# Performance work log

Hardware: AMD Instinct MI355X
Metric: run time of the kernel (lower is better)

Reference implementation:

```python
import jax, jax.numpy as jnp
import numpy as np

N, E, G = 16384, 65536, 64
IN_F, HID, MID, NCLS = 63, 2048, 1024, 18
EPS = 1e-5
SLOPE = 0.01  # default leaky_relu negative_slope


def setup_inputs() -> dict:
    key = jax.random.key(0)
    ks = jax.random.split(key, 24)
    p = lambda k, shp: jax.random.normal(k, shp, dtype=jnp.float32) * 0.02
    inp = {
        "h": jax.random.normal(ks[0], (N, IN_F), dtype=jnp.float32),
        "src": jax.random.randint(ks[1], (E,), 0, N, dtype=jnp.int32),
        "dst": jax.random.randint(ks[2], (E,), 0, N, dtype=jnp.int32),
        "graph_id": jnp.sort(jax.random.randint(ks[3], (N,), 0, G, dtype=jnp.int32)),
        # SAGEConv layers: fc_self W, fc_neigh W, bias
        "Ws1": p(ks[4], (IN_F, HID)), "Wn1": p(ks[5], (IN_F, HID)), "b1": jnp.zeros((HID,), jnp.float32),
        "Ws2": p(ks[6], (HID, HID)), "Wn2": p(ks[7], (HID, HID)), "b2": jnp.zeros((HID,), jnp.float32),
        "Ws3": p(ks[8], (HID, HID)), "Wn3": p(ks[9], (HID, HID)), "b3": jnp.zeros((HID,), jnp.float32),
        # BatchNorm affine params
        "g1": jnp.ones((HID,), jnp.float32), "be1": jnp.zeros((HID,), jnp.float32),
        "g2": jnp.ones((HID,), jnp.float32), "be2": jnp.zeros((HID,), jnp.float32),
        "g3": jnp.ones((HID,), jnp.float32), "be3": jnp.zeros((HID,), jnp.float32),
        # MLP head
        "fc1_w": p(ks[10], (HID, HID)), "fc1_b": jnp.zeros((HID,), jnp.float32),
        "fc2_w": p(ks[11], (HID, MID)), "fc2_b": jnp.zeros((MID,), jnp.float32),
        "fc3_w": p(ks[12], (MID, NCLS)), "fc3_b": jnp.zeros((NCLS,), jnp.float32),
    }
    return inp


def _sage_mean(h, src, dst, Ws, Wn, b):
    # DGL SAGEConv, aggregator='mean': rst = fc_self(h) + fc_neigh(mean_{u in N(v)} h_u) + bias
    deg = jax.ops.segment_sum(jnp.ones((E,), h.dtype), dst, num_segments=N)
    neigh_sum = jax.ops.segment_sum(h[src], dst, num_segments=N)  # [N, d_in]
    neigh_mean = neigh_sum / jnp.maximum(deg, 1.0)[:, None]       # zero-degree -> 0
    return h @ Ws + neigh_mean @ Wn + b


def _bn(x, gamma, beta):
    # BatchNorm1d in training mode: batch stats over node dim, biased variance
    mu = jnp.mean(x, axis=0)
    var = jnp.mean(jnp.square(x - mu), axis=0)
    return (x - mu) * jax.lax.rsqrt(var + EPS) * gamma + beta


def reference(h, src, dst, graph_id,
              Ws1, Wn1, b1, Ws2, Wn2, b2, Ws3, Wn3, b3,
              g1, be1, g2, be2, g3, be3,
              fc1_w, fc1_b, fc2_w, fc2_b, fc3_w, fc3_b):
    lrelu = lambda x: jax.nn.leaky_relu(x, SLOPE)
    h = lrelu(_bn(_sage_mean(h, src, dst, Ws1, Wn1, b1), g1, be1))
    h = lrelu(_bn(_sage_mean(h, src, dst, Ws2, Wn2, b2), g2, be2))
    h = lrelu(_bn(_sage_mean(h, src, dst, Ws3, Wn3, b3), g3, be3))
    # AvgPooling over batched graph (dropout = identity in eval)
    cnt = jax.ops.segment_sum(jnp.ones((N,), h.dtype), graph_id, num_segments=G)
    hg = jax.ops.segment_sum(h, graph_id, num_segments=G) / jnp.maximum(cnt, 1.0)[:, None]
    x = lrelu(hg @ fc1_w + fc1_b)
    x = lrelu(x @ fc2_w + fc2_b)
    return x @ fc3_w + fc3_b
```

## Files before the change

kernel.cpp:

```cpp
#include <hip/hip_runtime.h>
#include <hip/hip_bf16.h>

#define NN   16384
#define EE   65536
#define GG   64
#define INF  63
#define HID  2048
#define MID  1024
#define NCLS 18
#define EPS  1e-5f
#define SLOPE 0.01f
#define MR   (NN / 128)

typedef unsigned short ushort;
typedef unsigned int uint;

using bf16x8 = __attribute__((ext_vector_type(8))) __bf16;
using f32x4  = __attribute__((ext_vector_type(4))) float;

__device__ __forceinline__ ushort f2us(float x) {
    __hip_bfloat16 b = __float2bfloat16(x);
    return __builtin_bit_cast(ushort, b);
}
__device__ __forceinline__ float us2f(ushort u) {
    return __bfloat162float(__builtin_bit_cast(__hip_bfloat16, u));
}

__device__ __forceinline__ void gll16(const ushort* g, ushort* l) {
    __builtin_amdgcn_global_load_lds(
        (const __attribute__((address_space(1))) uint*)g,
        (__attribute__((address_space(3))) uint*)l, 16, 0, 0);
}


__global__ void k_zero_i(int* __restrict__ p, int n) {
    int i = blockIdx.x * blockDim.x + threadIdx.x;
    if (i < n) p[i] = 0;
}


__global__ void k_count(const int* __restrict__ dst, int* __restrict__ cnt) {
    int e = blockIdx.x * blockDim.x + threadIdx.x;
    if (e < EE) atomicAdd(&cnt[dst[e]], 1);
}

__global__ void k_scan(const int* __restrict__ cnt, int* __restrict__ off,
                       float* __restrict__ deg) {
    __shared__ int sh[1024];
    int t = threadIdx.x;
    int base = t * 16;
    int loc[16];
    int s = 0;
#pragma unroll
    for (int i = 0; i < 16; ++i) {
        int c = cnt[base + i];
        loc[i] = s;
        s += c;
        deg[base + i] = (float)c;
    }
    sh[t] = s;
    __syncthreads();
    for (int d = 1; d < 1024; d <<= 1) {
        int v = (t >= d) ? sh[t - d] : 0;
        __syncthreads();
        sh[t] += v;
        __syncthreads();
    }
    int excl = sh[t] - s;
#pragma unroll
    for (int i = 0; i < 16; ++i) off[base + i] = excl + loc[i];
    if (t == 1023) off[NN] = sh[1023];
}

__global__ void k_fill(const int* __restrict__ src, const int* __restrict__ dst,
                       const int* __restrict__ off, int* __restrict__ cur,
                       int* __restrict__ csr_src) {
    int e = blockIdx.x * blockDim.x + threadIdx.x;
    if (e < EE) {
        int d = dst[e];
        int p = atomicAdd(&cur[d], 1);
        csr_src[off[d] + p] = src[e];
    }
}


__global__ void k_h2bf_c(const float* __restrict__ h, ushort* __restrict__ Xc) {
    int i = blockIdx.x * 256 + threadIdx.x;
    int r = i >> 6, c = i & 63;
    Xc[(size_t)r * 128 + c] = (c < INF) ? f2us(h[(size_t)r * INF + c]) : (ushort)0;
}

__global__ void k_agg_small_c(const float* __restrict__ X, ushort* __restrict__ Xc,
                              const int* __restrict__ off, const int* __restrict__ csr_src,
                              const float* __restrict__ deg) {
    int v = blockIdx.x;
    int f = threadIdx.x;
    float acc = 0.f;
    if (f < INF) {
        int s = off[v], e = off[v + 1];
        for (int i = s; i < e; ++i) acc += X[(size_t)csr_src[i] * INF + f];
        acc /= fmaxf(deg[v], 1.f);
    }
    Xc[(size_t)v * 128 + 64 + f] = f2us(acc);
}


__global__ void k_aggbn(const ushort* __restrict__ Ybf,
                        const float* __restrict__ sc8, const float* __restrict__ sh8,
                        ushort* __restrict__ X, ushort* __restrict__ AggX,
                        const int* __restrict__ off, const int* __restrict__ csr_src,
                        const float* __restrict__ deg) {
    int v = blockIdx.x;
    int t = threadIdx.x;
    int c = t * 8;
    float sc[8], sh[8];
    *(float4*)&sc[0] = *(const float4*)&sc8[c];
    *(float4*)&sc[4] = *(const float4*)&sc8[c + 4];
    *(float4*)&sh[0] = *(const float4*)&sh8[c];
    *(float4*)&sh[4] = *(const float4*)&sh8[c + 4];

    {
        uint4 u = ((const uint4*)(Ybf + (size_t)v * HID))[t];
        uint wds[4] = {u.x, u.y, u.z, u.w};
        uint o[4];
#pragma unroll
        for (int j = 0; j < 4; ++j) {
            float a = sc[2 * j] * us2f((ushort)(wds[j] & 0xffffu)) + sh[2 * j];
            float b = sc[2 * j + 1] * us2f((ushort)(wds[j] >> 16)) + sh[2 * j + 1];
            a = a > 0.f ? a : SLOPE * a;
            b = b > 0.f ? b : SLOPE * b;
            o[j] = (uint)f2us(a) | ((uint)f2us(b) << 16);
        }
        ((uint4*)(X + (size_t)v * HID))[t] = make_uint4(o[0], o[1], o[2], o[3]);
    }

    int s = off[v], e = off[v + 1];
    float acc[8];
#pragma unroll
    for (int j = 0; j < 8; ++j) acc[j] = 0.f;
    for (int i = s; i < e; ++i) {
        uint4 u = ((const uint4*)(Ybf + (size_t)csr_src[i] * HID))[t];
        uint wds[4] = {u.x, u.y, u.z, u.w};
#pragma unroll
        for (int j = 0; j < 4; ++j) {
            float a = sc[2 * j] * us2f((ushort)(wds[j] & 0xffffu)) + sh[2 * j];
            float b = sc[2 * j + 1] * us2f((ushort)(wds[j] >> 16)) + sh[2 * j + 1];
            acc[2 * j]     += a > 0.f ? a : SLOPE * a;
            acc[2 * j + 1] += b > 0.f ? b : SLOPE * b;
        }
    }
    float inv = 1.f / fmaxf(deg[v], 1.f);
    uint o[4];
#pragma unroll
    for (int j = 0; j < 4; ++j)
        o[j] = (uint)f2us(acc[2 * j] * inv) | ((uint)f2us(acc[2 * j + 1] * inv) << 16);
    ((uint4*)(AggX + (size_t)v * HID))[t] = make_uint4(o[0], o[1], o[2], o[3]);
}


__global__ void k_wt2(const float* __restrict__ W0, const float* __restrict__ W1,
                      int K, int N, ushort* __restrict__ Wt0, ushort* __restrict__ Wt1,
                      int Kp) {
    const float* W = blockIdx.z ? W1 : W0;
    ushort* Wt = blockIdx.z ? Wt1 : Wt0;
    __shared__ float t[32][33];
    int kb = blockIdx.y * 32, nb = blockIdx.x * 32;
    int tx = threadIdx.x & 31, ty = threadIdx.x >> 5;
#pragma unroll
    for (int i = 0; i < 32; i += 8) {
        int k = kb + ty + i;
        t[ty + i][tx] = (k < K) ? W[(size_t)k * N + nb + tx] : 0.f;
// ... 14 lines not shown
#pragma unroll
    for (int i = 0; i < 32; i += 8) {
        int k = kb + ty + i;
        t[ty + i][tx] = (k < Kw) ? W[(size_t)k * N + nb + tx] : 0.f;
    }
    __syncthreads();
#pragma unroll
    for (int i = 0; i < 32; i += 8)
        Wtc[(size_t)(nb + ty + i) * KP + kOff + kb + tx] = f2us(t[tx][ty + i]);
}

__global__ void k_wt(const float* __restrict__ W, int K, int N,
                     ushort* __restrict__ Wt, int Kp) {
    __shared__ float t[32][33];
    int kb = blockIdx.y * 32, nb = blockIdx.x * 32;
    int tx = threadIdx.x & 31, ty = threadIdx.x >> 5;
#pragma unroll
    for (int i = 0; i < 32; i += 8) {
        int k = kb + ty + i;
        t[ty + i][tx] = (k < K) ? W[(size_t)k * N + nb + tx] : 0.f;
    }
    __syncthreads();
#pragma unroll
    for (int i = 0; i < 32; i += 8)
        Wt[(size_t)(nb + ty + i) * Kp + kb + tx] = f2us(t[tx][ty + i]);
}


#define BK 64

__global__ __launch_bounds__(256)
void k_mgemm(const ushort* __restrict__ A1, int lda1, const ushort* __restrict__ B1t, int ldb1, int K1,
             const ushort* __restrict__ A2, int lda2, const ushort* __restrict__ B2t, int ldb2, int K2,
             const float* __restrict__ bias, float* __restrict__ Cf, ushort* __restrict__ Cbf,
             int ldc, int fuse_lrelu, float* __restrict__ s1p, float* __restrict__ s2p,
             size_t cStrideZ) {
    __shared__ __align__(16) ushort As[128 * BK];
    __shared__ __align__(16) ushort Bs[128 * BK];
    __shared__ float sb1[4][64];
    __shared__ float sb2[4][64];
    const int tid = threadIdx.x;
    const int lane = tid & 63;
    const int w = tid >> 6;
    const int rowBase = blockIdx.y * 128;
    const int colBase = blockIdx.x * 128;
    const int m0 = (w & 1) * 64;
    const int n0 = (w >> 1) * 64;
    const int z = blockIdx.z;
    A1 += (size_t)z * K1;
    B1t += (size_t)z * K1;
    if (Cf) Cf += (size_t)z * cStrideZ;

    f32x4 acc[4][4];
#pragma unroll
    for (int mi = 0; mi < 4; ++mi)
#pragma unroll
        for (int ni = 0; ni < 4; ++ni) acc[mi][ni] = (f32x4){0.f, 0.f, 0.f, 0.f};

    const int lrow = w * 8 + (lane >> 3);
    const int gc8 = ((lane & 7) ^ (lane >> 3)) * 8;
    const int la = lane & 15, q = lane >> 4;
    const int la7 = lane & 7;

    for (int pass = 0; pass < 2; ++pass) {
        const ushort* A  = pass ? A2 : A1;
        const ushort* Bt = pass ? B2t : B1t;
        const int K   = pass ? K2 : K1;
        const int lda = pass ? lda2 : lda1;
        const int ldb = pass ? ldb2 : ldb1;
        if (A == nullptr) continue;
        const ushort* gA = A + (size_t)(rowBase + lrow) * lda + gc8;
        const ushort* gB = Bt + (size_t)(colBase + lrow) * ldb + gc8;
        for (int kt = 0; kt < K; kt += BK) {
#pragma unroll
            for (int j = 0; j < 4; ++j) {
                gll16(gA + (size_t)(j * 32) * lda + kt, As + j * 2048 + w * 512);
                gll16(gB + (size_t)(j * 32) * ldb + kt, Bs + j * 2048 + w * 512);
            }
            __syncthreads();
#pragma unroll
            for (int kk = 0; kk < 2; ++kk) {
                const int lc8 = ((kk * 4 + q) ^ la7) * 8;
                bf16x8 av[4], bv[4];
#pragma unroll
                for (int mi = 0; mi < 4; ++mi)
                    av[mi] = *(const bf16x8*)&As[(m0 + mi * 16 + la) * BK + lc8];
#pragma unroll
                for (int ni = 0; ni < 4; ++ni)
                    bv[ni] = *(const bf16x8*)&Bs[(n0 + ni * 16 + la) * BK + lc8];
#pragma unroll
                for (int mi = 0; mi < 4; ++mi)
#pragma unroll
                    for (int ni = 0; ni < 4; ++ni)
                        acc[mi][ni] = __builtin_amdgcn_mfma_f32_16x16x32_bf16(
                            av[mi], bv[ni], acc[mi][ni], 0, 0, 0);
            }
            __syncthreads();
        }
    }

#pragma unroll
    for (int mi = 0; mi < 4; ++mi) {
#pragma unroll
        for (int ni = 0; ni < 4; ++ni) {
            const int lc = colBase + n0 + ni * 16 + la;
            const float bv = bias ? bias[lc] : 0.f;
#pragma unroll
            for (int r = 0; r < 4; ++r) {
                const int row = rowBase + m0 + mi * 16 + q * 4 + r;
                float v = acc[mi][ni][r] + bv;
                if (fuse_lrelu) v = v > 0.f ? v : SLOPE * v;
                if (Cbf) Cbf[(size_t)row * ldc + lc] = f2us(v);
                else     Cf[(size_t)row * ldc + lc] = v;
            }
        }
    }

    if (s1p) {
#pragma unroll
        for (int ni = 0; ni < 4; ++ni) {
            const int lc = colBase + n0 + ni * 16 + la;
            const float bv = bias ? bias[lc] : 0.f;
            float t1 = 0.f, t2 = 0.f;
#pragma unroll
            for (int mi = 0; mi < 4; ++mi)
#pragma unroll
                for (int r = 0; r < 4; ++r) {
                    float v = acc[mi][ni][r] + bv;
                    t1 += v;
                    t2 += v * v;
                }
            t1 += __shfl_xor(t1, 16);
            t1 += __shfl_xor(t1, 32);
            t2 += __shfl_xor(t2, 16);
            t2 += __shfl_xor(t2, 32);
            if (q == 0) {
                sb1[w][ni * 16 + la] = t1;
                sb2[w][ni * 16 + la] = t2;
            }
        }
        __syncthreads();
        if (tid < 128) {
            int half = tid >> 6, j = tid & 63;
            float v1 = sb1[2 * half][j] + sb1[2 * half + 1][j];
            float v2 = sb2[2 * half][j] + sb2[2 * half + 1][j];
            size_t o = (size_t)blockIdx.y * ldc + colBase + half * 64 + j;
            s1p[o] = v1;
            s2p[o] = v2;
        }
    }
}


#define STAGEH(kti_, wh_) do {                                                 \
    int _kt = (kti_);                                                          \
    int _ktc = _kt < KT ? _kt : KT - 1;                                        \
    int _pass = (_ktc >= kt1);                                                 \
    int _k0 = (_ktc - (_pass ? kt1 : 0)) << 6;                                 \
    const ushort* _M;                                                          \
    int _h, _slot;                                                             \
    if ((wh_) == 0)      { _M = (_pass ? A2 : A1) + (size_t)rowBase * HID; _h = 0; _slot = 0; } \
    else if ((wh_) == 2) { _M = (_pass ? A2 : A1) + (size_t)rowBase * HID; _h = 1; _slot = 1; } \
    else if ((wh_) == 1) { _M = (_pass ? B2t : B1t) + (size_t)colBase * HID; _h = 0; _slot = 2; } \
    else                 { _M = (_pass ? B2t : B1t) + (size_t)colBase * HID; _h = 1; _slot = 3; } \
    const ushort* _g = _M + (size_t)(_h * 128 + srow) * HID + (size_t)(_k0 + sch); \
    ushort* _l = &lds[_kt & 1][_slot][0] + ldsl;                               \
    gll16(_g, _l);                                                             \
    gll16(_g + (size_t)64 * HID, _l + 4096);                                   \
} while (0)

#define PHASE(buf_, hm_, hn_, loadB_, skti_, swh_, wait_) do {                 \
    const ushort* _Ah = &lds[(buf_)][(hm_)][0];                                \
    if (loadB_) {                                                              \
        const ushort* _Bh = &lds[(buf_)][2 + (hn_)][0];                        \
        _Pragma("unroll")                                                      \
        for (int g_ = 0; g_ < 2; ++g_) {                                       \
            b[g_][0] = *(const bf16x8*)&_Bh[brb + g_ * 4096 + c0];             \
            b[g_][1] = *(const bf16x8*)&_Bh[brb + g_ * 4096 + c1];             \
        }                                                                      \
    }                                                                          \
    _Pragma("unroll")                                                          \
    for (int f_ = 0; f_ < 4; ++f_) {                                           \
        a[f_][0] = *(const bf16x8*)&_Ah[arb + f_ * 2048 + c0];                 \
        a[f_][1] = *(const bf16x8*)&_Ah[arb + f_ * 2048 + c1];                 \
    }                                                                          \
    STAGEH((skti_), (swh_));                                                   \
    __builtin_amdgcn_s_barrier();                                              \
    __builtin_amdgcn_s_setprio(1);                                             \
    _Pragma("unroll")                                                          \
    for (int kk_ = 0; kk_ < 2; ++kk_)                                          \
        _Pragma("unroll")                                                      \
        for (int f_ = 0; f_ < 4; ++f_)                                         \
            _Pragma("unroll")                                                  \
            for (int g_ = 0; g_ < 2; ++g_)                                     \
                acc[(hm_) * 4 + f_][(hn_) * 2 + g_] =                          \
                    __builtin_amdgcn_mfma_f32_16x16x32_bf16(                   \
                        a[f_][kk_], b[g_][kk_],                                \
                        acc[(hm_) * 4 + f_][(hn_) * 2 + g_], 0, 0, 0);         \
    __builtin_amdgcn_s_setprio(0);                                             \
    if (wait_) asm volatile("s_waitcnt vmcnt(6)" ::: "memory");                \
    __builtin_amdgcn_s_barrier();                                              \
} while (0)

__global__ __launch_bounds__(512, 2)
void k_mgemm256(const ushort* __restrict__ A1, const ushort* __restrict__ B1t,
                const ushort* __restrict__ A2, const ushort* __restrict__ B2t,
                int K1, int K2,
                const float* __restrict__ bias, ushort* __restrict__ Cbf,
                float* __restrict__ s1p, float* __restrict__ s2p) {
    __shared__ __align__(16) ushort lds[2][4][128 * 64];
    __shared__ float sb1[2][256];
    __shared__ float sb2[2][256];

    const int tid  = threadIdx.x;
    const int w    = tid >> 6, lane = tid & 63;
    const int la   = lane & 15, q = lane >> 4, la7 = lane & 7;
    const int wm   = w >> 2, wn = w & 3;

    const int nx  = gridDim.x;
    const int lin = blockIdx.y * nx + blockIdx.x;
    const int cpx = (nx * gridDim.y) >> 3;
    const int swz = (lin & 7) * cpx + (lin >> 3);
    const int bx  = swz & (nx - 1), by = swz / nx;
    const int rowBase = by * 256, colBase = bx * 256;

    const int kt1 = K1 >> 6;
    const int KT  = kt1 + (K2 >> 6);

    const int srow = tid >> 3;
    const int sch  = ((tid & 7) ^ (srow & 7)) << 3;
    const int ldsl = w << 9;

    const int arb = (wm * 16 + la) * 64;
    const int brb = (wn * 16 + la) * 64;
    const int c0  = ((0 + q) ^ la7) << 3;
    const int c1  = ((4 + q) ^ la7) << 3;

    f32x4 acc[8][4];
#pragma unroll
    for (int mi = 0; mi < 8; ++mi)
#pragma unroll
        for (int ni = 0; ni < 4; ++ni) acc[mi][ni] = (f32x4){0.f, 0.f, 0.f, 0.f};
    bf16x8 a[4][2], b[2][2];

    STAGEH(0, 0); STAGEH(0, 1); STAGEH(0, 2); STAGEH(0, 3);
    STAGEH(1, 0);
    asm volatile("s_waitcnt vmcnt(6)" ::: "memory");
    __builtin_amdgcn_s_barrier();

    for (int t = 0; t < KT; ++t) {
        const int bf_ = t & 1;
        PHASE(bf_, 0, 0, 1, t + 1, 1, 1);
        PHASE(bf_, 1, 0, 0, t + 1, 2, 1);
        PHASE(bf_, 0, 1, 1, t + 1, 3, 0);
        PHASE(bf_, 1, 1, 0, t + 2, 0, 1);
    }

    __syncthreads();

#pragma unroll
    for (int mi = 0; mi < 8; ++mi) {
        const int row = rowBase + (mi >> 2) * 128 + wm * 16 + (mi & 3) * 32 + q * 4;
#pragma unroll
        for (int ni = 0; ni < 4; ++ni) {
            const int col = colBase + (ni >> 1) * 128 + wn * 16 + (ni & 1) * 64 + la;
            const float bv = bias[col];
#pragma unroll
            for (int r = 0; r < 4; ++r) {
                float v = acc[mi][ni][r] + bv;
                Cbf[(size_t)(row + r) * HID + col] = f2us(v);
            }
        }
    }

#pragma unroll
    for (int ni = 0; ni < 4; ++ni) {
        const int cib = (ni >> 1) * 128 + wn * 16 + (ni & 1) * 64 + la;
        const float bv = bias[colBase + cib];
        float t1 = 0.f, t2 = 0.f;
#pragma unroll
        for (int mi = 0; mi < 8; ++mi)
#pragma unroll
            for (int r = 0; r < 4; ++r) {
                float v = acc[mi][ni][r] + bv;
                t1 += v;
                t2 += v * v;
            }
        t1 += __shfl_xor(t1, 16);
        t1 += __shfl_xor(t1, 32);
        t2 += __shfl_xor(t2, 16);
        t2 += __shfl_xor(t2, 32);
        if (q == 0) { sb1[wm][cib] = t1; sb2[wm][cib] = t2; }
    }
    __syncthreads();
    if (tid < 256) {
        size_t o = (size_t)by * HID + colBase + tid;
        s1p[o] = sb1[0][tid] + sb1[1][tid];
        s2p[o] = sb2[0][tid] + sb2[1][tid];
    }
}


__global__ void k_bn_finalize(const float* __restrict__ p1, const float* __restrict__ p2,
                              const float* __restrict__ gamma, const float* __restrict__ beta,
                              float* __restrict__ scale, float* __restrict__ shift, int nrb) {
    int c = blockIdx.x * 256 + threadIdx.x;
    if (c >= HID) return;
    float s1 = 0.f, s2 = 0.f;
    for (int rb = 0; rb < nrb; ++rb) {
        s1 += p1[(size_t)rb * HID + c];
        s2 += p2[(size_t)rb * HID + c];
    }
    float mean = s1 * (1.f / (float)NN);
    float var = s2 * (1.f / (float)NN) - mean * mean;
    var = fmaxf(var, 0.f);
    float sc = gamma[c] * rsqrtf(var + EPS);
    scale[c] = sc;
    shift[c] = beta[c] - mean * sc;
}


__global__ void k_poolbn(const ushort* __restrict__ Ybf,
                         const float* __restrict__ scale, const float* __restrict__ shift,
                         const int* __restrict__ gstart, ushort* __restrict__ hgbf) {
    int g = blockIdx.y;
    int col = blockIdx.x * 256 + threadIdx.x;
    if (g >= GG) {
        hgbf[(size_t)g * HID + col] = 0;
        return;
    }
    int s = gstart[g], e = gstart[g + 1];
    float sc = scale[col], sh = shift[col];
    float acc = 0.f;
    for (int n = s; n < e; ++n) {
        float v = sc * us2f(Ybf[(size_t)n * HID + col]) + sh;
        acc += v > 0.f ? v : SLOPE * v;
    }
    hgbf[(size_t)g * HID + col] = f2us(acc / fmaxf((float)(e - s), 1.f));
}

__global__ void k_gstart(const int* __restrict__ gid, int* __restrict__ gstart) {
    int g = threadIdx.x;
    if (g > GG) return;
    int lo = 0, hi = NN;
    while (lo < hi) {
        int mid = (lo + hi) >> 1;
        if (gid[mid] < g) lo = mid + 1; else hi = mid;
    }
    gstart[g] = lo;
}


__global__ void k_redhead(const float* __restrict__ part, int P, size_t strideZ,
                          const float* __restrict__ bias, int ldc,
                          ushort* __restrict__ obf, float* __restrict__ of, int n) {
    int i = blockIdx.x * 256 + threadIdx.x;
    if (i >= n) return;
    float s = 0.f;
    for (int p = 0; p < P; ++p) s += part[(size_t)p * strideZ + i];
    s += bias[i % ldc];
    s = s > 0.f ? s : SLOPE * s;
    if (obf) obf[i] = f2us(s);
    else     of[i] = s;
}

__global__ void k_fc3(const float* __restrict__ x2, const float* __restrict__ W,
                      const float* __restrict__ b, float* __restrict__ out) {
    int g = blockIdx.x;
    int tid = threadIdx.x;
    float part[NCLS];
#pragma unroll
    for (int c = 0; c < NCLS; ++c) part[c] = 0.f;
    for (int k = tid; k < MID; k += 256) {
        float x = x2[(size_t)g * MID + k];
        const float* wr = W + (size_t)k * NCLS;
#pragma unroll
        for (int c = 0; c < NCLS; ++c) part[c] += x * wr[c];
    }
    __shared__ float red[4][NCLS];
    int lane = tid & 63, w = tid >> 6;
#pragma unroll
    for (int c = 0; c < NCLS; ++c) {
        float v = part[c];
        for (int o = 32; o > 0; o >>= 1) v += __shfl_down(v, o, 64);
        if (lane == 0) red[w][c] = v;
    }
    __syncthreads();
    if (tid < NCLS)
        out[(size_t)g * NCLS + tid] = red[0][tid] + red[1][tid] + red[2][tid] + red[3][tid] + b[tid];
}


extern "C" void kernel_launch(void* const* d_in, const int* in_sizes, int n_in,
                              void* d_out, int out_size, void* d_ws, size_t ws_size,
                              hipStream_t stream) {
    const float* h        = (const float*)d_in[0];
    const int*   src      = (const int*)d_in[1];
    const int*   dst      = (const int*)d_in[2];
    const int*   graph_id = (const int*)d_in[3];
    const float* Ws1 = (const float*)d_in[4];
    const float* Wn1 = (const float*)d_in[5];
    const float* b1  = (const float*)d_in[6];
    const float* Ws2 = (const float*)d_in[7];
    const float* Wn2 = (const float*)d_in[8];
    const float* b2  = (const float*)d_in[9];
    const float* Ws3 = (const float*)d_in[10];
    const float* Wn3 = (const float*)d_in[11];
    const float* b3  = (const float*)d_in[12];
    const float* g1  = (const float*)d_in[13];
    const float* be1 = (const float*)d_in[14];
    const float* g2  = (const float*)d_in[15];
    const float* be2 = (const float*)d_in[16];
    const float* g3  = (const float*)d_in[17];
    const float* be3 = (const float*)d_in[18];
    const float* fc1_w = (const float*)d_in[19];
    const float* fc1_b = (const float*)d_in[20];
    const float* fc2_w = (const float*)d_in[21];
    const float* fc2_b = (const float*)d_in[22];
    const float* fc3_w = (const float*)d_in[23];
    const float* fc3_b = (const float*)d_in[24];
    float* out = (float*)d_out;

    size_t off_b = 0;
    auto alloc = [&](size_t bytes) -> void* {
        void* p = (char*)d_ws + off_b;
        off_b += (bytes + 255) & ~(size_t)255;
        return p;
    };
    ushort* Wt0    = (ushort*)alloc((size_t)2 * HID * HID * 2);
    ushort* Wt1    = Wt0 + (size_t)HID * HID;
    ushort* X      = (ushort*)alloc((size_t)NN * HID * 2);
    ushort* AggX   = (ushort*)alloc((size_t)NN * HID * 2);
    ushort* Ybf    = (ushort*)alloc((size_t)NN * HID * 2);
    float*  deg    = (float*)alloc((size_t)NN * 4);
    int*    csroff = (int*)alloc((size_t)(NN + 1) * 4);
    int*    cursor = (int*)alloc((size_t)NN * 4);
    int*    csrsrc = (int*)alloc((size_t)EE * 4);
    float*  p1     = (float*)alloc((size_t)MR * HID * 4);
    float*  p2     = (float*)alloc((size_t)MR * HID * 4);
    float*  bnsc   = (float*)alloc((size_t)HID * 4);
    float*  bnsh   = (float*)alloc((size_t)HID * 4);
    int*    gstart = (int*)alloc((size_t)(GG + 1) * 4);

    ushort* Xc128 = X;
    ushort* hgbf  = AggX;
    ushort* x1bf  = AggX + (size_t)128 * HID;
    float*  x2f   = (float*)(AggX + (size_t)2 * 128 * HID);
    float*  partF = (float*)(AggX + (size_t)3 * 128 * HID);

    k_zero_i<<<dim3(NN / 256), dim3(256), 0, stream>>>(cursor, NN);
    k_count<<<dim3(EE / 256), dim3(256), 0, stream>>>(dst, cursor);
    k_scan<<<dim3(1), dim3(1024), 0, stream>>>(cursor, csroff, deg);
    k_zero_i<<<dim3(NN / 256), dim3(256), 0, stream>>>(cursor, NN);
    k_fill<<<dim3(EE / 256), dim3(256), 0, stream>>>(src, dst, csroff, cursor, csrsrc);
    k_gstart<<<dim3(1), dim3(128), 0, stream>>>(graph_id, gstart);

    k_h2bf_c<<<dim3(NN * 64 / 256), dim3(256), 0, stream>>>(h, Xc128);
    k_agg_small_c<<<dim3(NN), dim3(64), 0, stream>>>(h, Xc128, csroff, csrsrc, deg);
    k_wt2c<<<dim3(HID / 32, 2, 2), dim3(256), 0, stream>>>(Ws1, Wn1, INF, HID, Wt0, 128);
    k_mgemm<<<dim3(HID / 128, NN / 128, 1), dim3(256), 0, stream>>>(
        Xc128, 128, Wt0, 128, 128,
        (const ushort*)nullptr, 0, (const ushort*)nullptr, 0, 0,
        b1, (float*)nullptr, Ybf, HID, 0, p1, p2, 0);
    k_bn_finalize<<<dim3(HID / 256), dim3(256), 0, stream>>>(p1, p2, g1, be1, bnsc, bnsh, MR);
    k_aggbn<<<dim3(NN), dim3(256), 0, stream>>>(Ybf, bnsc, bnsh, X, AggX, csroff, csrsrc, deg);

    k_wt2<<<dim3(HID / 32, HID / 32, 2), dim3(256), 0, stream>>>(Ws2, Wn2, HID, HID, Wt0, Wt1, HID);
    k_mgemm256<<<dim3(HID / 256, NN / 256), dim3(512), 0, stream>>>(
        X, Wt0, AggX, Wt1, HID, HID, b2, Ybf, p1, p2);
    k_bn_finalize<<<dim3(HID / 256), dim3(256), 0, stream>>>(p1, p2, g2, be2, bnsc, bnsh, NN / 256);
    k_aggbn<<<dim3(NN), dim3(256), 0, stream>>>(Ybf, bnsc, bnsh, X, AggX, csroff, csrsrc, deg);

    k_wt2<<<dim3(HID / 32, HID / 32, 2), dim3(256), 0, stream>>>(Ws3, Wn3, HID, HID, Wt0, Wt1, HID);
    k_mgemm256<<<dim3(HID / 256, NN / 256), dim3(512), 0, stream>>>(
        X, Wt0, AggX, Wt1, HID, HID, b3, Ybf, p1, p2);
    k_bn_finalize<<<dim3(HID / 256), dim3(256), 0, stream>>>(p1, p2, g3, be3, bnsc, bnsh, NN / 256);

    k_poolbn<<<dim3(HID / 256, 128), dim3(256), 0, stream>>>(Ybf, bnsc, bnsh, gstart, hgbf);

    k_wt<<<dim3(HID / 32, HID / 32), dim3(256), 0, stream>>>(fc1_w, HID, HID, Wt0, HID);
    k_wt<<<dim3(MID / 32, HID / 32), dim3(256), 0, stream>>>(fc2_w, HID, MID, Wt1, HID);
    k_mgemm<<<dim3(HID / 128, 1, 4), dim3(256), 0, stream>>>(
        hgbf, HID, Wt0, HID, HID / 4,
        (const ushort*)nullptr, 0, (const ushort*)nullptr, 0, 0,
        (const float*)nullptr, partF, (ushort*)nullptr, HID, 0,
        (float*)nullptr, (float*)nullptr, (size_t)128 * HID);
    k_redhead<<<dim3(128 * HID / 256), dim3(256), 0, stream>>>(
        partF, 4, (size_t)128 * HID, fc1_b, HID, x1bf, (float*)nullptr, 128 * HID);
    k_mgemm<<<dim3(MID / 128, 1, 4), dim3(256), 0, stream>>>(
        x1bf, HID, Wt1, HID, HID / 4,
        (const ushort*)nullptr, 0, (const ushort*)nullptr, 0, 0,
        (const float*)nullptr, partF, (ushort*)nullptr, MID, 0,
        (float*)nullptr, (float*)nullptr, (size_t)128 * MID);
    k_redhead<<<dim3(128 * MID / 256), dim3(256), 0, stream>>>(
        partF, 4, (size_t)128 * MID, fc2_b, MID, (ushort*)nullptr, x2f, 128 * MID);
    k_fc3<<<dim3(GG), dim3(256), 0, stream>>>(x2f, fc3_w, fc3_b, out);
}
```

Baseline: 1.118 ms.

## Switch main GEMM from 16x16x32 to 32x32x16 MFMA tiles

Rewrites the inner loop of the fused SAGE GEMM to use 32x32x16 bf16 MFMA instructions with a per-wave 64x32 sub-tile instead of 16x16x32 fragments. A and B fragments are loaded once per k-tile and reused across the four phases, and the epilogue and BN statistics reduction are remapped to the 32x32 accumulator layout. The aim is fewer LDS reads per flop and higher MFMA throughput per instruction. In exchange, register pressure rises because it holds more fragments at launch bounds of 512 threads with 2 blocks per SM.

After: 1.083 ms. 3.1% less time.

```diff
diff --git a/kernel.cpp b/kernel.cpp
--- a/kernel.cpp
+++ b/kernel.cpp
@@ -17,6 +17,7 @@
 
 using bf16x8 = __attribute__((ext_vector_type(8))) __bf16;
 using f32x4  = __attribute__((ext_vector_type(4))) float;
+using f32x16 = __attribute__((ext_vector_type(16))) float;
 
 __device__ __forceinline__ ushort f2us(float x) {
     __hip_bfloat16 b = __float2bfloat16(x);
@@ -354,39 +355,6 @@
     gll16(_g + (size_t)64 * HID, _l + 4096);                                   \
 } while (0)
 
-#define PHASE(buf_, hm_, hn_, loadB_, skti_, swh_, wait_) do {                 \
-    const ushort* _Ah = &lds[(buf_)][(hm_)][0];                                \
-    if (loadB_) {                                                              \
-        const ushort* _Bh = &lds[(buf_)][2 + (hn_)][0];                        \
-        _Pragma("unroll")                                                      \
-        for (int g_ = 0; g_ < 2; ++g_) {                                       \
-            b[g_][0] = *(const bf16x8*)&_Bh[brb + g_ * 4096 + c0];             \
-            b[g_][1] = *(const bf16x8*)&_Bh[brb + g_ * 4096 + c1];             \
-        }                                                                      \
-    }                                                                          \
-    _Pragma("unroll")                                                          \
-    for (int f_ = 0; f_ < 4; ++f_) {                                           \
-        a[f_][0] = *(const bf16x8*)&_Ah[arb + f_ * 2048 + c0];                 \
-        a[f_][1] = *(const bf16x8*)&_Ah[arb + f_ * 2048 + c1];                 \
-    }                                                                          \
-    STAGEH((skti_), (swh_));                                                   \
-    __builtin_amdgcn_s_barrier();                                              \
-    __builtin_amdgcn_s_setprio(1);                                             \
-    _Pragma("unroll")                                                          \
-    for (int kk_ = 0; kk_ < 2; ++kk_)                                          \
-        _Pragma("unroll")                                                      \
-        for (int f_ = 0; f_ < 4; ++f_)                                         \
-            _Pragma("unroll")                                                  \
-            for (int g_ = 0; g_ < 2; ++g_)                                     \
-                acc[(hm_) * 4 + f_][(hn_) * 2 + g_] =                          \
-                    __builtin_amdgcn_mfma_f32_16x16x32_bf16(                   \
-                        a[f_][kk_], b[g_][kk_],                                \
-                        acc[(hm_) * 4 + f_][(hn_) * 2 + g_], 0, 0, 0);         \
-    __builtin_amdgcn_s_setprio(0);                                             \
-    if (wait_) asm volatile("s_waitcnt vmcnt(6)" ::: "memory");                \
-    __builtin_amdgcn_s_barrier();                                              \
-} while (0)
-
 __global__ __launch_bounds__(512, 2)
 void k_mgemm256(const ushort* __restrict__ A1, const ushort* __restrict__ B1t,
                 const ushort* __restrict__ A2, const ushort* __restrict__ B2t,
@@ -399,7 +367,7 @@
 
     const int tid  = threadIdx.x;
     const int w    = tid >> 6, lane = tid & 63;
-    const int la   = lane & 15, q = lane >> 4, la7 = lane & 7;
+    const int la31 = lane & 31, hi = lane >> 5, la7 = lane & 7;
     const int wm   = w >> 2, wn = w & 3;
 
     const int nx  = gridDim.x;
@@ -416,17 +384,19 @@
     const int sch  = ((tid & 7) ^ (srow & 7)) << 3;
     const int ldsl = w << 9;
 
-    const int arb = (wm * 16 + la) * 64;
-    const int brb = (wn * 16 + la) * 64;
-    const int c0  = ((0 + q) ^ la7) << 3;
-    const int c1  = ((4 + q) ^ la7) << 3;
-
-    f32x4 acc[8][4];
-#pragma unroll
-    for (int mi = 0; mi < 8; ++mi)
-#pragma unroll
-        for (int ni = 0; ni < 4; ++ni) acc[mi][ni] = (f32x4){0.f, 0.f, 0.f, 0.f};
-    bf16x8 a[4][2], b[2][2];
+    const int aoff = (wm * 64 + la31) * 64;
+    const int boff = (wn * 32 + la31) * 64;
+    int cofs[4];
+#pragma unroll
+    for (int s_ = 0; s_ < 4; ++s_)
+        cofs[s_] = (((s_ * 2 + hi) ^ la7) << 3);
+
+    f32x16 acc[8];
+#pragma unroll
+    for (int i = 0; i < 8; ++i)
+#pragma unroll
+        for (int r = 0; r < 16; ++r) acc[i][r] = 0.f;
+    bf16x8 aL[2][4], aH[2][4], bL[4], bH[4];
 
     STAGEH(0, 0); STAGEH(0, 1); STAGEH(0, 2); STAGEH(0, 3);
     STAGEH(1, 0);
@@ -435,47 +405,112 @@
 
     for (int t = 0; t < KT; ++t) {
         const int bf_ = t & 1;
-        PHASE(bf_, 0, 0, 1, t + 1, 1, 1);
-        PHASE(bf_, 1, 0, 0, t + 1, 2, 1);
-        PHASE(bf_, 0, 1, 1, t + 1, 3, 0);
-        PHASE(bf_, 1, 1, 0, t + 2, 0, 1);
+        const ushort* A0h = &lds[bf_][0][0];
+        const ushort* A1h = &lds[bf_][1][0];
+        const ushort* B0h = &lds[bf_][2][0];
+        const ushort* B1h = &lds[bf_][3][0];
+
+#pragma unroll
+        for (int m_ = 0; m_ < 2; ++m_)
+#pragma unroll
+            for (int s_ = 0; s_ < 4; ++s_)
+                aL[m_][s_] = *(const bf16x8*)&A0h[aoff + m_ * 2048 + cofs[s_]];
+#pragma unroll
+        for (int s_ = 0; s_ < 4; ++s_)
+            bL[s_] = *(const bf16x8*)&B0h[boff + cofs[s_]];
+        STAGEH(t + 1, 1);
+        __builtin_amdgcn_s_barrier();
+        __builtin_amdgcn_s_setprio(1);
+#pragma unroll
+        for (int s_ = 0; s_ < 4; ++s_)
+#pragma unroll
+            for (int m_ = 0; m_ < 2; ++m_)
+                acc[m_ * 2] = __builtin_amdgcn_mfma_f32_32x32x16_bf16(
+                    aL[m_][s_], bL[s_], acc[m_ * 2], 0, 0, 0);
+        __builtin_amdgcn_s_setprio(0);
+        asm volatile("s_waitcnt vmcnt(6)" ::: "memory");
+        __builtin_amdgcn_s_barrier();
+
+#pragma unroll
+        for (int m_ = 0; m_ < 2; ++m_)
+#pragma unroll
+            for (int s_ = 0; s_ < 4; ++s_)
+                aH[m_][s_] = *(const bf16x8*)&A1h[aoff + m_ * 2048 + cofs[s_]];
+        STAGEH(t + 1, 2);
+        __builtin_amdgcn_s_barrier();
+        __builtin_amdgcn_s_setprio(1);
+#pragma unroll
+        for (int s_ = 0; s_ < 4; ++s_)
+#pragma unroll
+            for (int m_ = 0; m_ < 2; ++m_)
+                acc[4 + m_ * 2] = __builtin_amdgcn_mfma_f32_32x32x16_bf16(
+                    aH[m_][s_], bL[s_], acc[4 + m_ * 2], 0, 0, 0);
+        __builtin_amdgcn_s_setprio(0);
+        asm volatile("s_waitcnt vmcnt(6)" ::: "memory");
+        __builtin_amdgcn_s_barrier();
+
+#pragma unroll
+        for (int s_ = 0; s_ < 4; ++s_)
+            bH[s_] = *(const bf16x8*)&B1h[boff + cofs[s_]];
+        STAGEH(t + 1, 3);
+        __builtin_amdgcn_s_barrier();
+        __builtin_amdgcn_s_setprio(1);
+#pragma unroll
+        for (int s_ = 0; s_ < 4; ++s_)
+#pragma unroll
+            for (int m_ = 0; m_ < 2; ++m_)
+                acc[1 + m_ * 2] = __builtin_amdgcn_mfma_f32_32x32x16_bf16(
+                    aL[m_][s_], bH[s_], acc[1 + m_ * 2], 0, 0, 0);
+        __builtin_amdgcn_s_setprio(0);
+        __builtin_amdgcn_s_barrier();
+
+        STAGEH(t + 2, 0);
+        __builtin_amdgcn_s_barrier();
+        __builtin_amdgcn_s_setprio(1);
+#pragma unroll
+        for (int s_ = 0; s_ < 4; ++s_)
+#pragma unroll
+            for (int m_ = 0; m_ < 2; ++m_)
+                acc[5 + m_ * 2] = __builtin_amdgcn_mfma_f32_32x32x16_bf16(
+                    aH[m_][s_], bH[s_], acc[5 + m_ * 2], 0, 0, 0);
+        __builtin_amdgcn_s_setprio(0);
+        asm volatile("s_waitcnt vmcnt(6)" ::: "memory");
+        __builtin_amdgcn_s_barrier();
     }
 
     __syncthreads();
 
 #pragma unroll
-    for (int mi = 0; mi < 8; ++mi) {
-        const int row = rowBase + (mi >> 2) * 128 + wm * 16 + (mi & 3) * 32 + q * 4;
-#pragma unroll
-        for (int ni = 0; ni < 4; ++ni) {
-            const int col = colBase + (ni >> 1) * 128 + wn * 16 + (ni & 1) * 64 + la;
+    for (int mt = 0; mt < 4; ++mt) {
+        const int rb = rowBase + (mt >> 1) * 128 + wm * 64 + (mt & 1) * 32 + hi * 4;
+#pragma unroll
+        for (int nt = 0; nt < 2; ++nt) {
+            const int col = colBase + nt * 128 + wn * 32 + la31;
             const float bv = bias[col];
 #pragma unroll
-            for (int r = 0; r < 4; ++r) {
-                float v = acc[mi][ni][r] + bv;
-                Cbf[(size_t)(row + r) * HID + col] = f2us(v);
+            for (int r = 0; r < 16; ++r) {
+                const int row = rb + (r & 3) + (r >> 2) * 8;
+                Cbf[(size_t)row * HID + col] = f2us(acc[mt * 2 + nt][r] + bv);
             }
         }
     }
 
 #pragma unroll
-    for (int ni = 0; ni < 4; ++ni) {
-        const int cib = (ni >> 1) * 128 + wn * 16 + (ni & 1) * 64 + la;
-        const float bv = bias[colBase + cib];
+    for (int nt = 0; nt < 2; ++nt) {
+        const int cl = nt * 128 + wn * 32 + la31;
+        const float bv = bias[colBase + cl];
         float t1 = 0.f, t2 = 0.f;
 #pragma unroll
-        for (int mi = 0; mi < 8; ++mi)
-#pragma unroll
-            for (int r = 0; r < 4; ++r) {
-                float v = acc[mi][ni][r] + bv;
+        for (int mt = 0; mt < 4; ++mt)
+#pragma unroll
+            for (int r = 0; r < 16; ++r) {
+                float v = acc[mt * 2 + nt][r] + bv;
                 t1 += v;
                 t2 += v * v;
             }
-        t1 += __shfl_xor(t1, 16);
         t1 += __shfl_xor(t1, 32);
-        t2 += __shfl_xor(t2, 16);
         t2 += __shfl_xor(t2, 32);
-        if (q == 0) { sb1[wm][cib] = t1; sb2[wm][cib] = t2; }
+        if (hi == 0) { sb1[wm][cl] = t1; sb2[wm][cl] = t2; }
     }
     __syncthreads();
     if (tid < 256) {
```

## Keep A fragments in registers across GEMM phases and use running staging pointers

Applied to the files above, without the earlier changes.

Restructures the main loop of the 256x256 bf16 GEMM so that the low and high A fragments are each read from LDS once per k-tile and kept in registers for two MFMA phases, instead of being re-read in every phase. The per-stage global address computation (clamping, pass selection, branch on half) is replaced by four incrementing pointers, with a one-time jump from the first operand pair to the second at the K1 boundary. The loop is unrolled by two so LDS buffer indices become compile-time constants. This cuts LDS traffic and scalar address math, at the cost of more live VGPRs. It also drops the clamp on the last prefetch, so the final tiles can issue loads past the valid K range.

Result: faster. 1.064 ms (-4.8%).

```diff
diff --git a/kernel.cpp b/kernel.cpp
--- a/kernel.cpp
+++ b/kernel.cpp
@@ -337,54 +337,99 @@
 }
 
 
-#define STAGEH(kti_, wh_) do {                                                 \
-    int _kt = (kti_);                                                          \
-    int _ktc = _kt < KT ? _kt : KT - 1;                                        \
-    int _pass = (_ktc >= kt1);                                                 \
-    int _k0 = (_ktc - (_pass ? kt1 : 0)) << 6;                                 \
-    const ushort* _M;                                                          \
-    int _h, _slot;                                                             \
-    if ((wh_) == 0)      { _M = (_pass ? A2 : A1) + (size_t)rowBase * HID; _h = 0; _slot = 0; } \
-    else if ((wh_) == 2) { _M = (_pass ? A2 : A1) + (size_t)rowBase * HID; _h = 1; _slot = 1; } \
-    else if ((wh_) == 1) { _M = (_pass ? B2t : B1t) + (size_t)colBase * HID; _h = 0; _slot = 2; } \
-    else                 { _M = (_pass ? B2t : B1t) + (size_t)colBase * HID; _h = 1; _slot = 3; } \
-    const ushort* _g = _M + (size_t)(_h * 128 + srow) * HID + (size_t)(_k0 + sch); \
-    ushort* _l = &lds[_kt & 1][_slot][0] + ldsl;                               \
-    gll16(_g, _l);                                                             \
-    gll16(_g + (size_t)64 * HID, _l + 4096);                                   \
+#define STG(ptr_, dst_) do {                                                   \
+    gll16((ptr_), (dst_) + ldsl);                                              \
+    gll16((ptr_) + (size_t)64 * HID, (dst_) + ldsl + 4096);                    \
 } while (0)
 
-#define PHASE(buf_, hm_, hn_, loadB_, skti_, swh_, wait_) do {                 \
-    const ushort* _Ah = &lds[(buf_)][(hm_)][0];                                \
-    if (loadB_) {                                                              \
-        const ushort* _Bh = &lds[(buf_)][2 + (hn_)][0];                        \
-        _Pragma("unroll")                                                      \
-        for (int g_ = 0; g_ < 2; ++g_) {                                       \
-            b[g_][0] = *(const bf16x8*)&_Bh[brb + g_ * 4096 + c0];             \
-            b[g_][1] = *(const bf16x8*)&_Bh[brb + g_ * 4096 + c1];             \
-        }                                                                      \
+#define DO_TILE(BUF) do {                                                      \
+    if (tcur + 1 == kt1) { rB0 += dB; rA1 += dA; rB1 += dB; }                  \
+    if (tcur + 2 == kt1) { rA0 += dA; }                                        \
+    const ushort* A0h = &lds[BUF][0][0];                                       \
+    const ushort* A1h = &lds[BUF][1][0];                                       \
+    const ushort* B0h = &lds[BUF][2][0];                                       \
+    const ushort* B1h = &lds[BUF][3][0];                                       \
+                                                             \
+    _Pragma("unroll")                                                          \
+    for (int f_ = 0; f_ < 4; ++f_) {                                           \
+        aL[f_][0] = *(const bf16x8*)&A0h[arb + f_ * 2048 + c0];                \
+        aL[f_][1] = *(const bf16x8*)&A0h[arb + f_ * 2048 + c1];                \
     }                                                                          \
     _Pragma("unroll")                                                          \
-    for (int f_ = 0; f_ < 4; ++f_) {                                           \
-        a[f_][0] = *(const bf16x8*)&_Ah[arb + f_ * 2048 + c0];                 \
-        a[f_][1] = *(const bf16x8*)&_Ah[arb + f_ * 2048 + c1];                 \
+    for (int g_ = 0; g_ < 2; ++g_) {                                           \
+        bL[g_][0] = *(const bf16x8*)&B0h[brb + g_ * 4096 + c0];                \
+        bL[g_][1] = *(const bf16x8*)&B0h[brb + g_ * 4096 + c1];                \
     }                                                                          \
-    STAGEH((skti_), (swh_));                                                   \
+    STG(rB0, &lds[(BUF) ^ 1][2][0]);                                           \
     __builtin_amdgcn_s_barrier();                                              \
     __builtin_amdgcn_s_setprio(1);                                             \
     _Pragma("unroll")                                                          \
-    for (int kk_ = 0; kk_ < 2; ++kk_)                                          \
+    for (int kk = 0; kk < 2; ++kk)                                             \
         _Pragma("unroll")                                                      \
         for (int f_ = 0; f_ < 4; ++f_)                                         \
             _Pragma("unroll")                                                  \
             for (int g_ = 0; g_ < 2; ++g_)                                     \
-                acc[(hm_) * 4 + f_][(hn_) * 2 + g_] =                          \
-                    __builtin_amdgcn_mfma_f32_16x16x32_bf16(                   \
-                        a[f_][kk_], b[g_][kk_],                                \
-                        acc[(hm_) * 4 + f_][(hn_) * 2 + g_], 0, 0, 0);         \
+                acc[f_][g_] = __builtin_amdgcn_mfma_f32_16x16x32_bf16(         \
+                    aL[f_][kk], bL[g_][kk], acc[f_][g_], 0, 0, 0);             \
     __builtin_amdgcn_s_setprio(0);                                             \
-    if (wait_) asm volatile("s_waitcnt vmcnt(6)" ::: "memory");                \
+    asm volatile("s_waitcnt vmcnt(6)" ::: "memory");                           \
     __builtin_amdgcn_s_barrier();                                              \
+                                                             \
+    _Pragma("unroll")                                                          \
+    for (int f_ = 0; f_ < 4; ++f_) {                                           \
+        aH[f_][0] = *(const bf16x8*)&A1h[arb + f_ * 2048 + c0];                \
+        aH[f_][1] = *(const bf16x8*)&A1h[arb + f_ * 2048 + c1];                \
+    }                                                                          \
+    STG(rA1, &lds[(BUF) ^ 1][1][0]);                                           \
+    __builtin_amdgcn_s_barrier();                                              \
+    __builtin_amdgcn_s_setprio(1);                                             \
+    _Pragma("unroll")                                                          \
+    for (int kk = 0; kk < 2; ++kk)                                             \
+        _Pragma("unroll")                                                      \
+        for (int f_ = 0; f_ < 4; ++f_)                                         \
+            _Pragma("unroll")                                                  \
+            for (int g_ = 0; g_ < 2; ++g_)                                     \
+                acc[4 + f_][g_] = __builtin_amdgcn_mfma_f32_16x16x32_bf16(     \
+                    aH[f_][kk], bL[g_][kk], acc[4 + f_][g_], 0, 0, 0);         \
+    __builtin_amdgcn_s_setprio(0);                                             \
+    asm volatile("s_waitcnt vmcnt(6)" ::: "memory");                           \
+    __builtin_amdgcn_s_barrier();                                              \
+                                                             \
+    _Pragma("unroll")                                                          \
+    for (int g_ = 0; g_ < 2; ++g_) {                                           \
+        bH[g_][0] = *(const bf16x8*)&B1h[brb + g_ * 4096 + c0];                \
+        bH[g_][1] = *(const bf16x8*)&B1h[brb + g_ * 4096 + c1];                \
+    }                                                                          \
+    STG(rB1, &lds[(BUF) ^ 1][3][0]);                                           \
+    __builtin_amdgcn_s_barrier();                                              \
+    __builtin_amdgcn_s_setprio(1);                                             \
+    _Pragma("unroll")                                                          \
+    for (int kk = 0; kk < 2; ++kk)                                             \
+        _Pragma("unroll")                                                      \
+        for (int f_ = 0; f_ < 4; ++f_)                                         \
+            _Pragma("unroll")                                                  \
+            for (int g_ = 0; g_ < 2; ++g_)                                     \
+                acc[f_][2 + g_] = __builtin_amdgcn_mfma_f32_16x16x32_bf16(     \
+                    aL[f_][kk], bH[g_][kk], acc[f_][2 + g_], 0, 0, 0);         \
+    __builtin_amdgcn_s_setprio(0);                                             \
+    __builtin_amdgcn_s_barrier();                                              \
+                                                             \
+    STG(rA0, &lds[BUF][0][0]);                                                 \
+    __builtin_amdgcn_s_barrier();                                              \
+    __builtin_amdgcn_s_setprio(1);                                             \
+    _Pragma("unroll")                                                          \
+    for (int kk = 0; kk < 2; ++kk)                                             \
+        _Pragma("unroll")                                                      \
+        for (int f_ = 0; f_ < 4; ++f_)                                         \
+            _Pragma("unroll")                                                  \
+            for (int g_ = 0; g_ < 2; ++g_)                                     \
+                acc[4 + f_][2 + g_] = __builtin_amdgcn_mfma_f32_16x16x32_bf16( \
+                    aH[f_][kk], bH[g_][kk], acc[4 + f_][2 + g_], 0, 0, 0);     \
+    __builtin_amdgcn_s_setprio(0);                                             \
+    asm volatile("s_waitcnt vmcnt(6)" ::: "memory");                           \
+    __builtin_amdgcn_s_barrier();                                              \
+    rA0 += 64; rB0 += 64; rA1 += 64; rB1 += 64;                                \
+    ++tcur;                                                                    \
 } while (0)
 
 __global__ __launch_bounds__(512, 2)
@@ -416,6 +461,13 @@
     const int sch  = ((tid & 7) ^ (srow & 7)) << 3;
     const int ldsl = w << 9;
 
+    const ushort* rA0 = A1 + (size_t)(rowBase + srow) * HID + sch;
+    const ushort* rA1 = A1 + (size_t)(rowBase + 128 + srow) * HID + sch;
+    const ushort* rB0 = B1t + (size_t)(colBase + srow) * HID + sch;
+    const ushort* rB1 = B1t + (size_t)(colBase + 128 + srow) * HID + sch;
+    const ptrdiff_t dA = (A2 - A1) - K1;
+    const ptrdiff_t dB = (B2t - B1t) - K1;
+
     const int arb = (wm * 16 + la) * 64;
     const int brb = (wn * 16 + la) * 64;
     const int c0  = ((0 + q) ^ la7) << 3;
@@ -426,19 +478,21 @@
     for (int mi = 0; mi < 8; ++mi)
 #pragma unroll
         for (int ni = 0; ni < 4; ++ni) acc[mi][ni] = (f32x4){0.f, 0.f, 0.f, 0.f};
-    bf16x8 a[4][2], b[2][2];
-
-    STAGEH(0, 0); STAGEH(0, 1); STAGEH(0, 2); STAGEH(0, 3);
-    STAGEH(1, 0);
+    bf16x8 aL[4][2], aH[4][2], bL[2][2], bH[2][2];
+
+    STG(rA0, &lds[0][0][0]); rA0 += 64;
+    STG(rB0, &lds[0][2][0]);
+    STG(rA1, &lds[0][1][0]);
+    STG(rB1, &lds[0][3][0]);
+    STG(rA0, &lds[1][0][0]); rA0 += 64;
+    rB0 += 64; rA1 += 64; rB1 += 64;
     asm volatile("s_waitcnt vmcnt(6)" ::: "memory");
     __builtin_amdgcn_s_barrier();
 
-    for (int t = 0; t < KT; ++t) {
-        const int bf_ = t & 1;
-        PHASE(bf_, 0, 0, 1, t + 1, 1, 1);
-        PHASE(bf_, 1, 0, 0, t + 1, 2, 1);
-        PHASE(bf_, 0, 1, 1, t + 1, 3, 0);
-        PHASE(bf_, 1, 1, 0, t + 2, 0, 1);
+    int tcur = 0;
+    for (int it = 0; it < KT; it += 2) {
+        DO_TILE(0);
+        DO_TILE(1);
     }
 
     __syncthreads();
```

## Shrink fused SAGE GEMM to 128x128 tiles with simpler double-buffered pipeline

Applied to the files above, without the earlier changes.

Rewrites the two-input SAGE GEMM kernel to use 128x128 output tiles with 256 threads instead of 256x256 with 512 threads. The four quarter-tile phases per K step are replaced by one phase per K tile, double-buffered in LDS, with pointer-increment staging that switches from the self operand to the neighbour operand at the K1 boundary. This gives a larger grid and smaller LDS and register footprint, which should allow more resident blocks and better load balance across CUs. The cost is lower arithmetic intensity per tile, so global and L2 traffic goes up. The BN partial-sum row count is adjusted to match the new tile height.

After: 1.099 ms. About the same (-1.7%).

```diff
diff --git a/kernel.cpp b/kernel.cpp
--- a/kernel.cpp
+++ b/kernel.cpp
@@ -337,77 +337,75 @@
 }
 
 
-#define STAGEH(kti_, wh_) do {                                                 \
-    int _kt = (kti_);                                                          \
-    int _ktc = _kt < KT ? _kt : KT - 1;                                        \
-    int _pass = (_ktc >= kt1);                                                 \
-    int _k0 = (_ktc - (_pass ? kt1 : 0)) << 6;                                 \
-    const ushort* _M;                                                          \
-    int _h, _slot;                                                             \
-    if ((wh_) == 0)      { _M = (_pass ? A2 : A1) + (size_t)rowBase * HID; _h = 0; _slot = 0; } \
-    else if ((wh_) == 2) { _M = (_pass ? A2 : A1) + (size_t)rowBase * HID; _h = 1; _slot = 1; } \
-    else if ((wh_) == 1) { _M = (_pass ? B2t : B1t) + (size_t)colBase * HID; _h = 0; _slot = 2; } \
-    else                 { _M = (_pass ? B2t : B1t) + (size_t)colBase * HID; _h = 1; _slot = 3; } \
-    const ushort* _g = _M + (size_t)(_h * 128 + srow) * HID + (size_t)(_k0 + sch); \
-    ushort* _l = &lds[_kt & 1][_slot][0] + ldsl;                               \
-    gll16(_g, _l);                                                             \
-    gll16(_g + (size_t)64 * HID, _l + 4096);                                   \
+#define STG8(pa_, pb_) do {                                                    \
+    gll16((pa_), &lds[sb_][0][0] + ldsl);                                      \
+    gll16((pa_) + (size_t)32 * HID, &lds[sb_][0][0] + ldsl + 2048);            \
+    gll16((pa_) + (size_t)64 * HID, &lds[sb_][0][0] + ldsl + 4096);            \
+    gll16((pa_) + (size_t)96 * HID, &lds[sb_][0][0] + ldsl + 6144);            \
+    gll16((pb_), &lds[sb_][1][0] + ldsl);                                      \
+    gll16((pb_) + (size_t)32 * HID, &lds[sb_][1][0] + ldsl + 2048);            \
+    gll16((pb_) + (size_t)64 * HID, &lds[sb_][1][0] + ldsl + 4096);            \
+    gll16((pb_) + (size_t)96 * HID, &lds[sb_][1][0] + ldsl + 6144);            \
 } while (0)
 
-#define PHASE(buf_, hm_, hn_, loadB_, skti_, swh_, wait_) do {                 \
-    const ushort* _Ah = &lds[(buf_)][(hm_)][0];                                \
-    if (loadB_) {                                                              \
-        const ushort* _Bh = &lds[(buf_)][2 + (hn_)][0];                        \
-        _Pragma("unroll")                                                      \
-        for (int g_ = 0; g_ < 2; ++g_) {                                       \
-            b[g_][0] = *(const bf16x8*)&_Bh[brb + g_ * 4096 + c0];             \
-            b[g_][1] = *(const bf16x8*)&_Bh[brb + g_ * 4096 + c1];             \
-        }                                                                      \
+#define DO_TILE(BUF) do {                                                      \
+    if (tcur + 2 == kt1) { rA += dA; rB += dB; }                               \
+    const ushort* Ah = &lds[BUF][0][0];                                        \
+    const ushort* Bh = &lds[BUF][1][0];                                        \
+    bf16x8 af[4][2], bf[4][2];                                                 \
+    _Pragma("unroll")                                                          \
+    for (int f_ = 0; f_ < 4; ++f_) {                                           \
+        af[f_][0] = *(const bf16x8*)&Ah[arb + f_ * 1024 + c0];                 \
+        af[f_][1] = *(const bf16x8*)&Ah[arb + f_ * 1024 + c1];                 \
     }                                                                          \
     _Pragma("unroll")                                                          \
-    for (int f_ = 0; f_ < 4; ++f_) {                                           \
-        a[f_][0] = *(const bf16x8*)&_Ah[arb + f_ * 2048 + c0];                 \
-        a[f_][1] = *(const bf16x8*)&_Ah[arb + f_ * 2048 + c1];                 \
+    for (int g_ = 0; g_ < 4; ++g_) {                                           \
+        bf[g_][0] = *(const bf16x8*)&Bh[brb + g_ * 1024 + c0];                 \
+        bf[g_][1] = *(const bf16x8*)&Bh[brb + g_ * 1024 + c1];                 \
     }                                                                          \
-    STAGEH((skti_), (swh_));                                                   \
-    __builtin_amdgcn_s_barrier();                                              \
+    asm volatile("s_waitcnt lgkmcnt(0)" ::: "memory");                         \
+    __builtin_amdgcn_s_barrier();    \
+    {                                                                          \
+        const int sb_ = BUF;                                                   \
+        STG8(rA, rB);                       \
+    }                                                                          \
     __builtin_amdgcn_s_setprio(1);                                             \
     _Pragma("unroll")                                                          \
-    for (int kk_ = 0; kk_ < 2; ++kk_)                                          \
+    for (int kk = 0; kk < 2; ++kk)                                             \
         _Pragma("unroll")                                                      \
         for (int f_ = 0; f_ < 4; ++f_)                                         \
             _Pragma("unroll")                                                  \
-            for (int g_ = 0; g_ < 2; ++g_)                                     \
-                acc[(hm_) * 4 + f_][(hn_) * 2 + g_] =                          \
-                    __builtin_amdgcn_mfma_f32_16x16x32_bf16(                   \
-                        a[f_][kk_], b[g_][kk_],                                \
-                        acc[(hm_) * 4 + f_][(hn_) * 2 + g_], 0, 0, 0);         \
+            for (int g_ = 0; g_ < 4; ++g_)                                     \
+                acc[f_][g_] = __builtin_amdgcn_mfma_f32_16x16x32_bf16(         \
+                    af[f_][kk], bf[g_][kk], acc[f_][g_], 0, 0, 0);             \
     __builtin_amdgcn_s_setprio(0);                                             \
-    if (wait_) asm volatile("s_waitcnt vmcnt(6)" ::: "memory");                \
-    __builtin_amdgcn_s_barrier();                                              \
+    asm volatile("s_waitcnt vmcnt(8)" ::: "memory");                           \
+    __builtin_amdgcn_s_barrier();                        \
+    rA += 64; rB += 64;                                                        \
+    ++tcur;                                                                    \
 } while (0)
 
-__global__ __launch_bounds__(512, 2)
+__global__ __launch_bounds__(256, 2)
 void k_mgemm256(const ushort* __restrict__ A1, const ushort* __restrict__ B1t,
                 const ushort* __restrict__ A2, const ushort* __restrict__ B2t,
                 int K1, int K2,
                 const float* __restrict__ bias, ushort* __restrict__ Cbf,
                 float* __restrict__ s1p, float* __restrict__ s2p) {
-    __shared__ __align__(16) ushort lds[2][4][128 * 64];
-    __shared__ float sb1[2][256];
-    __shared__ float sb2[2][256];
+    __shared__ __align__(16) ushort lds[2][2][128 * 64];
+    __shared__ float sb1[2][128];
+    __shared__ float sb2[2][128];
 
     const int tid  = threadIdx.x;
     const int w    = tid >> 6, lane = tid & 63;
     const int la   = lane & 15, q = lane >> 4, la7 = lane & 7;
-    const int wm   = w >> 2, wn = w & 3;
+    const int wm   = w >> 1, wn = w & 1;
 
     const int nx  = gridDim.x;
     const int lin = blockIdx.y * nx + blockIdx.x;
     const int cpx = (nx * gridDim.y) >> 3;
     const int swz = (lin & 7) * cpx + (lin >> 3);
     const int bx  = swz & (nx - 1), by = swz / nx;
-    const int rowBase = by * 256, colBase = bx * 256;
+    const int rowBase = by * 128, colBase = bx * 128;
 
     const int kt1 = K1 >> 6;
     const int KT  = kt1 + (K2 >> 6);
@@ -416,39 +414,49 @@
     const int sch  = ((tid & 7) ^ (srow & 7)) << 3;
     const int ldsl = w << 9;
 
-    const int arb = (wm * 16 + la) * 64;
-    const int brb = (wn * 16 + la) * 64;
+    const ushort* rA = A1 + (size_t)(rowBase + srow) * HID + sch;
+    const ushort* rB = B1t + (size_t)(colBase + srow) * HID + sch;
+    const ptrdiff_t dA = (A2 - A1) - K1;
+    const ptrdiff_t dB = (B2t - B1t) - K1;
+
+    const int arb = (wm * 64 + la) * 64;
+    const int brb = (wn * 64 + la) * 64;
     const int c0  = ((0 + q) ^ la7) << 3;
     const int c1  = ((4 + q) ^ la7) << 3;
 
-    f32x4 acc[8][4];
-#pragma unroll
-    for (int mi = 0; mi < 8; ++mi)
+    f32x4 acc[4][4];
+#pragma unroll
+    for (int mi = 0; mi < 4; ++mi)
 #pragma unroll
         for (int ni = 0; ni < 4; ++ni) acc[mi][ni] = (f32x4){0.f, 0.f, 0.f, 0.f};
-    bf16x8 a[4][2], b[2][2];
-
-    STAGEH(0, 0); STAGEH(0, 1); STAGEH(0, 2); STAGEH(0, 3);
-    STAGEH(1, 0);
-    asm volatile("s_waitcnt vmcnt(6)" ::: "memory");
+
+    {
+        const int sb_ = 0;
+        STG8(rA, rB);
+    }
+    rA += 64; rB += 64;
+    {
+        const int sb_ = 1;
+        STG8(rA, rB);
+    }
+    rA += 64; rB += 64;
+    asm volatile("s_waitcnt vmcnt(8)" ::: "memory");
     __builtin_amdgcn_s_barrier();
 
-    for (int t = 0; t < KT; ++t) {
-        const int bf_ = t & 1;
-        PHASE(bf_, 0, 0, 1, t + 1, 1, 1);
-        PHASE(bf_, 1, 0, 0, t + 1, 2, 1);
-        PHASE(bf_, 0, 1, 1, t + 1, 3, 0);
-        PHASE(bf_, 1, 1, 0, t + 2, 0, 1);
+    int tcur = 0;
+    for (int it = 0; it < KT; it += 2) {
+        DO_TILE(0);
+        DO_TILE(1);
     }
 
     __syncthreads();
 
 #pragma unroll
-    for (int mi = 0; mi < 8; ++mi) {
-        const int row = rowBase + (mi >> 2) * 128 + wm * 16 + (mi & 3) * 32 + q * 4;
+    for (int mi = 0; mi < 4; ++mi) {
+        const int row = rowBase + wm * 64 + mi * 16 + q * 4;
 #pragma unroll
         for (int ni = 0; ni < 4; ++ni) {
-            const int col = colBase + (ni >> 1) * 128 + wn * 16 + (ni & 1) * 64 + la;
+            const int col = colBase + wn * 64 + ni * 16 + la;
             const float bv = bias[col];
 #pragma unroll
             for (int r = 0; r < 4; ++r) {
@@ -460,11 +468,11 @@
 
 #pragma unroll
     for (int ni = 0; ni < 4; ++ni) {
-        const int cib = (ni >> 1) * 128 + wn * 16 + (ni & 1) * 64 + la;
+        const int cib = wn * 64 + ni * 16 + la;
         const float bv = bias[colBase + cib];
         float t1 = 0.f, t2 = 0.f;
 #pragma unroll
-        for (int mi = 0; mi < 8; ++mi)
+        for (int mi = 0; mi < 4; ++mi)
 #pragma unroll
             for (int r = 0; r < 4; ++r) {
                 float v = acc[mi][ni][r] + bv;
@@ -478,7 +486,7 @@
         if (q == 0) { sb1[wm][cib] = t1; sb2[wm][cib] = t2; }
     }
     __syncthreads();
-    if (tid < 256) {
+    if (tid < 128) {
         size_t o = (size_t)by * HID + colBase + tid;
         s1p[o] = sb1[0][tid] + sb1[1][tid];
         s2p[o] = sb2[0][tid] + sb2[1][tid];
@@ -651,15 +659,15 @@
     k_aggbn<<<dim3(NN), dim3(256), 0, stream>>>(Ybf, bnsc, bnsh, X, AggX, csroff, csrsrc, deg);
 
     k_wt2<<<dim3(HID / 32, HID / 32, 2), dim3(256), 0, stream>>>(Ws2, Wn2, HID, HID, Wt0, Wt1, HID);
-    k_mgemm256<<<dim3(HID / 256, NN / 256), dim3(512), 0, stream>>>(
+    k_mgemm256<<<dim3(HID / 128, NN / 128), dim3(256), 0, stream>>>(
         X, Wt0, AggX, Wt1, HID, HID, b2, Ybf, p1, p2);
-    k_bn_finalize<<<dim3(HID / 256), dim3(256), 0, stream>>>(p1, p2, g2, be2, bnsc, bnsh, NN / 256);
+    k_bn_finalize<<<dim3(HID / 256), dim3(256), 0, stream>>>(p1, p2, g2, be2, bnsc, bnsh, MR);
     k_aggbn<<<dim3(NN), dim3(256), 0, stream>>>(Ybf, bnsc, bnsh, X, AggX, csroff, csrsrc, deg);
 
     k_wt2<<<dim3(HID / 32, HID / 32, 2), dim3(256), 0, stream>>>(Ws3, Wn3, HID, HID, Wt0, Wt1, HID);
-    k_mgemm256<<<dim3(HID / 256, NN / 256), dim3(512), 0, stream>>>(
+    k_mgemm256<<<dim3(HID / 128, NN / 128), dim3(256), 0, stream>>>(
         X, Wt0, AggX, Wt1, HID, HID, b3, Ybf, p1, p2);
-    k_bn_finalize<<<dim3(HID / 256), dim3(256), 0, stream>>>(p1, p2, g3, be3, bnsc, bnsh, NN / 256);
+    k_bn_finalize<<<dim3(HID / 256), dim3(256), 0, stream>>>(p1, p2, g3, be3, bnsc, bnsh, MR);
 
     k_poolbn<<<dim3(HID / 256, 128), dim3(256), 0, stream>>>(Ybf, bnsc, bnsh, gstart, hgbf);
 
```
